# Kernel optimization log

Hardware: AMD Instinct MI355X
Metric: run time of the kernel (lower is better)

## Reference

```python
import jax, jax.numpy as jnp
import numpy as np

N, E, C, ED = 50000, 800000, 128, 16
NEG_SLOPE = 0.2


def setup_inputs() -> dict:
    key = jax.random.key(0)
    ks = jax.random.split(key, 18)
    inp = {
        "h": jax.random.normal(ks[0], (N, C), jnp.float32),
        "edge_index": jax.random.randint(ks[1], (2, E), 0, N),
        "edge_attr": jax.random.normal(ks[2], (E, ED), jnp.float32),
        "reducible": jax.random.randint(ks[3], (N,), 0, 2) > 0,
    }
    names = ["W", "att_src", "att_dst", "W_edge", "att_edge", "W_res", "bias"]
    shapes = [(C, C), (C,), (C,), (ED, C), (C,), (C, C), (C,)]
    i = 4
    for pre in ["red_", "irr_"]:
        for n, sh in zip(names, shapes):
            inp[pre + n] = jax.random.normal(ks[i], sh, jnp.float32) * 0.05
            i += 1
    return inp


def _gat_conv(h, src, dst, edge_attr, W, att_src, att_dst, W_edge, att_edge, W_res, bias):
    """PyG GATConv (heads=1, residual=True, add_self_loops=True, fill_value='mean')."""
    n = h.shape[0]
    # self-loop edge_attr = mean of incoming edge_attr per node (0 if none)
    sum_attr = jax.ops.segment_sum(edge_attr, dst, num_segments=n)
    cnt = jax.ops.segment_sum(jnp.ones((edge_attr.shape[0],), edge_attr.dtype), dst, num_segments=n)
    mean_attr = sum_attr / jnp.maximum(cnt, 1.0)[:, None]
    loop = jnp.arange(n)
    s = jnp.concatenate([src, loop])   # [E+N]
    d = jnp.concatenate([dst, loop])   # [E+N]
    ea = jnp.concatenate([edge_attr, mean_attr], axis=0)  # [E+N, ED]
    x = h @ W                              # [N, C]
    a_src = x @ att_src                    # [N]
    a_dst = x @ att_dst                    # [N]
    a_edge = (ea @ W_edge) @ att_edge      # [E+N]
    alpha = jax.nn.leaky_relu(a_src[s] + a_dst[d] + a_edge, NEG_SLOPE)
    # per-destination softmax (every node has a self-loop -> denom > 0)
    m = jax.ops.segment_max(alpha, d, num_segments=n)
    ex = jnp.exp(alpha - m[d])
    denom = jax.ops.segment_sum(ex, d, num_segments=n)
    w = ex / denom[d]                      # [E+N]
    out = jax.ops.segment_sum(w[:, None] * x[s], d, num_segments=n)  # [N, C]
    return out + h @ W_res + bias


def reference(h, edge_index, edge_attr, reducible,
              red_W, red_att_src, red_att_dst, red_W_edge, red_att_edge, red_W_res, red_bias,
              irr_W, irr_att_src, irr_att_dst, irr_W_edge, irr_att_edge, irr_W_res, irr_bias):
    src, dst = edge_index[0], edge_index[1]
    out_r = _gat_conv(h, src, dst, edge_attr, red_W, red_att_src, red_att_dst,
                      red_W_edge, red_att_edge, red_W_res, red_bias)
    out_i = _gat_conv(h, src, dst, edge_attr, irr_W, irr_att_src, irr_att_dst,
                      irr_W_edge, irr_att_edge, irr_W_res, irr_bias)
    return jax.nn.relu(jnp.where(reducible[:, None], out_r, out_i))
```

## Files before the change

kernel.cpp:

```cpp
#include <hip/hip_runtime.h>
#include <hip/hip_bf16.h>

#define CDIM 128
#define EDIM 16
#define NEG_SLOPE 0.2f

typedef __attribute__((ext_vector_type(8))) short bf16x8;
typedef __attribute__((ext_vector_type(4))) float f32x4;
typedef __attribute__((ext_vector_type(2))) float f32x2;
typedef unsigned int uint;
typedef unsigned short ushort;

__device__ __forceinline__ ushort f2bf(float f) {
    uint u = __float_as_uint(f);
    return (ushort)((u + 0x7fffu + ((u >> 16) & 1u)) >> 16);
}
__device__ __forceinline__ uint packbf(float lo, float hi) {
    return ((uint)f2bf(hi) << 16) | (uint)f2bf(lo);
}
__device__ __forceinline__ float bflo(uint w) { return __uint_as_float(w << 16); }
__device__ __forceinline__ float bfhi(uint w) { return __uint_as_float(w & 0xffff0000u); }

__device__ __forceinline__ bool redtest(const void* red, int i, int notInt, int notFloat) {
    if (!notInt)        return ((const int*)red)[i] != 0;
    else if (!notFloat) return ((const float*)red)[i] != 0.f;
    else                return ((const unsigned char*)red)[i] != 0;
}

__global__ void bcatwe_kernel(const float* __restrict__ Wr, const float* __restrict__ Wi,
                              const float* __restrict__ Wrr, const float* __restrict__ Wri,
                              ushort* __restrict__ BT,
                              const float* __restrict__ WeR, const float* __restrict__ aeR,
                              const float* __restrict__ WeI, const float* __restrict__ aeI,
                              float* __restrict__ we) {
    if (blockIdx.x < 256) {
        int idx = blockIdx.x * 256 + threadIdx.x;
        int c = idx >> 7, k = idx & 127;
        const float* srcm;
        if (c < 128)      srcm = Wr;
        else if (c < 256) srcm = Wi;
        else if (c < 384) srcm = Wrr;
        else              srcm = Wri;
        BT[idx] = f2bf(srcm[k * 128 + (c & 127)]);
    } else {
        int lane = threadIdx.x;
        if (lane < 16) {
            float s = 0.f;
            for (int c = 0; c < CDIM; ++c) s += WeR[lane * CDIM + c] * aeR[c];
            we[lane] = s;
        } else if (lane < 32) {
            int j = lane - 16;
            float s = 0.f;
            for (int c = 0; c < CDIM; ++c) s += WeI[j * CDIM + c] * aeI[c];
            we[16 + j] = s;
        }
    }
}

__global__ __launch_bounds__(256) void prep_kernel(const uint* __restrict__ red, int nwords,
                                                   int* __restrict__ flags,
                                                   const int* __restrict__ dst, int* __restrict__ cnt,
                                                   int* __restrict__ rank,
                                                   const float* __restrict__ ea, const float* __restrict__ we,
                                                   uint* __restrict__ escal4,
                                                   const float* __restrict__ h, ushort* __restrict__ hbf,
                                                   int E, int n4) {
    int i = blockIdx.x * 256 + threadIdx.x;
    if (i < nwords) {
        uint w = red[i];
        bool isInt = (w <= 1u);
        bool isFloat = (w == 0u) || (w == 0x3f800000u);
        if (!isInt) atomicOr(&flags[0], 1);
        if (!isFloat) atomicOr(&flags[1], 1);
    }
    if (i < E) {
        int r = atomicAdd(&cnt[dst[i]], 1);
        __builtin_nontemporal_store(r, rank + i);
        const f32x4* row = (const f32x4*)(ea + (size_t)i * EDIM);
        const float4* we4 = (const float4*)we;
        float er = 0.f, ei = 0.f;
#pragma unroll
        for (int q = 0; q < 4; ++q) {
            f32x4 v = __builtin_nontemporal_load(row + q);
            float4 wr = we4[q], wi = we4[4 + q];
            er += v.x * wr.x + v.y * wr.y + v.z * wr.z + v.w * wr.w;
            ei += v.x * wi.x + v.y * wi.y + v.z * wi.z + v.w * wi.w;
        }
        __builtin_nontemporal_store(packbf(er, ei), escal4 + i);
    }
    if (i < n4) {
        f32x4 v = __builtin_nontemporal_load((const f32x4*)h + i);
        uint2 o;
        o.x = packbf(v.x, v.y);
        o.y = packbf(v.z, v.w);
        ((uint2*)hbf)[i] = o;
    }
}

__global__ __launch_bounds__(256) void gemm_dots(const ushort* __restrict__ A,
                                                 const ushort* __restrict__ BT,
                                                 ushort* __restrict__ C,
                                                 const float* __restrict__ attsr, const float* __restrict__ attdr,
                                                 const float* __restrict__ attsi, const float* __restrict__ attdi,
                                                 float* __restrict__ asr, float* __restrict__ adr,
                                                 float* __restrict__ asi, float* __restrict__ adi,
                                                 const void* __restrict__ red, const int* __restrict__ flags,
                                                 int M) {
    __shared__ ushort As[128 * 128];
    __shared__ ushort Bs[128 * 128];
    __shared__ float dots[2][128];
    __shared__ unsigned char redrow[128];
    int t = threadIdx.x;
    int lane = t & 63, wv = t >> 6;
    int rb = blockIdx.x * 128, cb = blockIdx.y * 128;
    int by = blockIdx.y;

    if (t < 128) { dots[0][t] = 0.f; dots[1][t] = 0.f; }
    if (by >= 2 && t < 128) {
        int gr = rb + t;
        int notInt = flags[0], notFloat = flags[1];
        redrow[t] = (gr < M) ? (redtest(red, gr, notInt, notFloat) ? 1 : 0) : 0;
    }

    int rsub = wv * 4 + (lane >> 4);
    int c0 = lane & 15;
#pragma unroll
    for (int p = 0; p < 8; ++p) {
        int row = p * 16 + rsub;
        int chunk = c0 ^ (row & 7);
        int gra = rb + row; if (gra > M - 1) gra = M - 1;
        const ushort* ga = A + (size_t)gra * 128 + chunk * 8;
        __builtin_amdgcn_global_load_lds(
            (const __attribute__((address_space(1))) void*)ga,
            (__attribute__((address_space(3))) void*)((char*)As + p * 4096 + wv * 1024),
            16, 0, 0);
        const ushort* gb = BT + (size_t)(cb + row) * 128 + chunk * 8;
        __builtin_amdgcn_global_load_lds(
            (const __attribute__((address_space(1))) void*)gb,
            (__attribute__((address_space(3))) void*)((char*)Bs + p * 4096 + wv * 1024),
            16, 0, 0);
    }
    __syncthreads();

    int wr = wv >> 1, wc = wv & 1;
    int l15 = lane & 15, l4 = lane >> 4;
    f32x4 acc[4][4];
#pragma unroll
    for (int i = 0; i < 4; ++i)
#pragma unroll
        for (int j = 0; j < 4; ++j) acc[i][j] = (f32x4){0.f, 0.f, 0.f, 0.f};

    const char* Ab = (const char*)As;
    const char* Bb = (const char*)Bs;
#pragma unroll
    for (int ks = 0; ks < 4; ++ks) {
        bf16x8 a[4], b[4];
#pragma unroll
        for (int f = 0; f < 4; ++f) {
            int row = wr * 64 + f * 16 + l15;
            int ch = (ks * 4 + l4) ^ (row & 7);
            a[f] = *(const bf16x8*)(Ab + row * 256 + ch * 16);
            int col = wc * 64 + f * 16 + l15;
            int ch2 = (ks * 4 + l4) ^ (col & 7);
            b[f] = *(const bf16x8*)(Bb + col * 256 + ch2 * 16);
        }
#pragma unroll
        for (int i = 0; i < 4; ++i)
#pragma unroll
            for (int j = 0; j < 4; ++j)
                acc[i][j] = __builtin_amdgcn_mfma_f32_16x16x32_bf16(a[i], b[j], acc[i][j], 0, 0, 0);
    }

    if (by < 2) {
        const float* attS = by ? attsi : attsr;
        const float* attD = by ? attdi : attdr;
        float aS[4], aD[4];
#pragma unroll
        for (int j = 0; j < 4; ++j) {
            int c = wc * 64 + j * 16 + l15;
            aS[j] = attS[c]; aD[j] = attD[c];
        }
#pragma unroll
        for (int i = 0; i < 4; ++i)
#pragma unroll
            for (int rr = 0; rr < 4; ++rr) {
                float ps = 0.f, pd = 0.f;
#pragma unroll
                for (int j = 0; j < 4; ++j) {
                    float v = acc[i][j][rr];
                    ps += v * aS[j]; pd += v * aD[j];
                }
#pragma unroll
                for (int d = 1; d < 16; d <<= 1) {
                    ps += __shfl_xor(ps, d); pd += __shfl_xor(pd, d);
                }
                if (l15 == 0) {
                    int row = wr * 64 + i * 16 + l4 * 4 + rr;
                    atomicAdd(&dots[0][row], ps);
                    atomicAdd(&dots[1][row], pd);
                }
            }
    }

#pragma unroll
    for (int i = 0; i < 4; ++i) {
        int rl = wr * 64 + i * 16 + l4 * 4;
#pragma unroll
        for (int j = 0; j < 4; ++j) {
            int col = cb + wc * 64 + j * 16 + l15;
#pragma unroll
            for (int r = 0; r < 4; ++r) {
                int gr = rb + rl + r;
                bool doit = gr < M;
                if (by == 2) doit = doit && redrow[rl + r];
                else if (by == 3) doit = doit && !redrow[rl + r];
                if (doit) C[(size_t)gr * 512 + col] = f2bf(acc[i][j][r]);
            }
        }
    }

    if (by < 2) {
        __syncthreads();
        if (t < 128) {
            int gr = rb + t;
            if (gr < M) {
                if (by == 0) { asr[gr] = dots[0][t]; adr[gr] = dots[1][t]; }
                else         { asi[gr] = dots[0][t]; adi[gr] = dots[1][t]; }
            }
        }
    }
}

__global__ __launch_bounds__(256) void scanA_kernel(const int* __restrict__ cnt,
                                                    int* __restrict__ offA,
                                                    int* __restrict__ bsum, int n) {
    __shared__ int wsum[4];
    int t = threadIdx.x, lane = t & 63, wid = t >> 6;
    int i0 = blockIdx.x * 1024 + t * 4;
    int v[4];
#pragma unroll
    for (int j = 0; j < 4; ++j) { int i = i0 + j; v[j] = (i < n) ? cnt[i] : 0; }
    int s = v[0] + v[1] + v[2] + v[3];
    int incl = s;
#pragma unroll
    for (int d = 1; d < 64; d <<= 1) { int u = __shfl_up(incl, d); if (lane >= d) incl += u; }
    if (lane == 63) wsum[wid] = incl;
    __syncthreads();
    int wpre = 0;
    for (int w = 0; w < wid; ++w) wpre += wsum[w];
    int run = wpre + incl - s;
#pragma unroll
    for (int j = 0; j < 4; ++j) {
        int i = i0 + j;
        if (i < n) offA[i] = run;
        run += v[j];
    }
    if (t == 255) bsum[blockIdx.x] = wpre + incl;
}

__global__ void scanB_kernel(int* __restrict__ bsum, int nb) {
    int lane = threadIdx.x;
    int carry = 0;
    for (int base = 0; base < nb; base += 64) {
        int i = base + lane;
        int v = (i < nb) ? bsum[i] : 0;
        int incl = v;
#pragma unroll
        for (int d = 1; d < 64; d <<= 1) { int u = __shfl_up(incl, d); if (lane >= d) incl += u; }
        if (i < nb) bsum[i] = carry + incl - v;
        carry += __shfl(incl, 63);
    }
}

__global__ __launch_bounds__(256) void scatter_kernel(
    const int* __restrict__ src, const int* __restrict__ dst,
    const int* __restrict__ rank, const uint* __restrict__ escal4,
    const void* __restrict__ red, const int* __restrict__ flags,
    const int* __restrict__ offA, const int* __restrict__ bsum,
    uint* __restrict__ csr, int E) {
    int e = blockIdx.x * 256 + threadIdx.x;
    if (e >= E) return;
    int s = __builtin_nontemporal_load(src + e);
    int d = __builtin_nontemporal_load(dst + e);
    uint ee = __builtin_nontemporal_load(escal4 + e);
    int rk = __builtin_nontemporal_load(rank + e);
    int notInt = flags[0], notFloat = flags[1];
    bool rr = redtest(red, d, notInt, notFloat);
    uint evb = rr ? (ee & 0xffffu) : (ee >> 16);
    int off = offA[d] + bsum[d >> 10];
    csr[off + rk] = (uint)s | (evb << 16);
}

__global__ __launch_bounds__(256) void node_kernel(
    const ushort* __restrict__ xcat,
    const float* __restrict__ adst_r, const float* __restrict__ adst_i,
    const float* __restrict__ asrc_r, const float* __restrict__ asrc_i,
    const void* __restrict__ red, const int* __restrict__ flags,
    const int* __restrict__ offA, const int* __restrict__ bsum,
    const uint* __restrict__ csr,
    const float* __restrict__ bias_r, const float* __restrict__ bias_i,
    float* __restrict__ out, int n, int E) {
    __shared__ uint2 buf[4][64];
    int wv = threadIdx.x >> 6, lane = threadIdx.x & 63;
    int node = blockIdx.x * 4 + wv;
    if (node >= n) return;

    int notInt = flags[0], notFloat = flags[1];
    bool r = redtest(red, node, notInt, notFloat);

    const float* asrc = r ? asrc_r : asrc_i;
    float adst = (r ? adst_r : adst_i)[node];
    uint vsel = r ? 0u : 256u;
    int b0 = offA[node] + bsum[node >> 10];
    int b1 = (node + 1 < n) ? (offA[node + 1] + bsum[(node + 1) >> 10]) : E;
    int k = b1 - b0;
    const char* xb = (const char*)xcat;
    uint lane4 = lane * 4;

    float m = -1e30f, denom = 0.f;
    float2 acca = make_float2(0.f, 0.f), accb = make_float2(0.f, 0.f);
    float sumE = 0.f;

    for (int base = b0; base < b1; base += 64) {
        int j = base + lane;
        float al = -1e30f; uint soff = 0;
        if (j < b1) {
            uint rec = __builtin_nontemporal_load(csr + j);
            uint s = rec & 0xffffu;
            float ev = bfhi(rec);
            sumE += ev;
            soff = s * 1024u + vsel;
            float a = asrc[s] + ev + adst;
            al = (a >= 0.f) ? a : NEG_SLOPE * a;
        }
        float cm = al;
#pragma unroll
        for (int d = 32; d; d >>= 1) cm = fmaxf(cm, __shfl_xor(cm, d));
        float mn = fmaxf(m, cm);
        float sc = __expf(m - mn);
        denom *= sc;
        acca.x *= sc; acca.y *= sc; accb.x *= sc; accb.y *= sc;
        m = mn;
        float ex = (j < b1) ? __expf(al - mn) : 0.f;
        buf[wv][lane] = make_uint2(__float_as_uint(ex), soff);
        __builtin_amdgcn_wave_barrier();
        int cc = min(64, b1 - base);
        int ccp = (cc + 7) & ~7;
        for (int tq = 0; tq < ccp; tq += 8) {
            uint2 u[8];
#pragma unroll
            for (int q = 0; q < 8; ++q) u[q] = buf[wv][tq + q];
            uint v[8];
#pragma unroll
            for (int q = 0; q < 8; ++q) v[q] = *(const uint*)(xb + u[q].y + lane4);
#pragma unroll
            for (int q = 0; q < 4; ++q) {
                float w = __uint_as_float(u[q].x);
                acca.x += w * bflo(v[q]); acca.y += w * bfhi(v[q]);
            }
#pragma unroll
            for (int q = 4; q < 8; ++q) {
                float w = __uint_as_float(u[q].x);
                accb.x += w * bflo(v[q]); accb.y += w * bfhi(v[q]);
            }
        }
        float exs = ex;
#pragma unroll
        for (int d = 32; d; d >>= 1) exs += __shfl_xor(exs, d);
        denom += exs;
        __builtin_amdgcn_wave_barrier();
    }
    float acc0 = acca.x + accb.x, acc1 = acca.y + accb.y;

#pragma unroll
    for (int d = 32; d; d >>= 1) sumE += __shfl_xor(sumE, d);
    float eself = sumE / fmaxf((float)k, 1.f);
    float a = asrc[node] + adst + eself;
    float aself = (a >= 0.f) ? a : NEG_SLOPE * a;
    float mn = fmaxf(m, aself);
    float sc = __expf(m - mn);
    float exl = __expf(aself - mn);
    denom = denom * sc + exl;
    uint voff = (uint)node * 1024u + vsel;
    uint vsw = *(const uint*)(xb + voff + lane4);
    acc0 = acc0 * sc + exl * bflo(vsw);
    acc1 = acc1 * sc + exl * bfhi(vsw);

    float inv = 1.f / denom;
    uint roff = (uint)node * 1024u + (r ? 512u : 768u);
    uint bw = *(const uint*)(xb + roff + lane4);
    float2 bi2 = ((const float2*)(r ? bias_r : bias_i))[lane];
    f32x2 o;
    o.x = fmaxf(acc0 * inv + bflo(bw) + bi2.x, 0.f);
    o.y = fmaxf(acc1 * inv + bfhi(bw) + bi2.y, 0.f);
    __builtin_nontemporal_store(o, ((f32x2*)out) + (size_t)node * 64 + lane);
}

extern "C" void kernel_launch(void* const* d_in, const int* in_sizes, int n_in,
                              void* d_out, int out_size, void* d_ws, size_t ws_size,
                              hipStream_t stream) {
    const float* h          = (const float*)d_in[0];
    const int*   edge_index = (const int*)d_in[1];
    const float* edge_attr  = (const float*)d_in[2];
    const void*  reducible  = d_in[3];
    const float* red_W      = (const float*)d_in[4];
    const float* red_att_src= (const float*)d_in[5];
    const float* red_att_dst= (const float*)d_in[6];
    const float* red_W_edge = (const float*)d_in[7];
    const float* red_att_edge=(const float*)d_in[8];
    const float* red_W_res  = (const float*)d_in[9];
    const float* red_bias   = (const float*)d_in[10];
    const float* irr_W      = (const float*)d_in[11];
    const float* irr_att_src= (const float*)d_in[12];
    const float* irr_att_dst= (const float*)d_in[13];
    const float* irr_W_edge = (const float*)d_in[14];
    const float* irr_att_edge=(const float*)d_in[15];
    const float* irr_W_res  = (const float*)d_in[16];
    const float* irr_bias   = (const float*)d_in[17];

    const int N = in_sizes[0] / CDIM;
    const int E = in_sizes[1] / 2;
    const int* src = edge_index;
    const int* dst = edge_index + E;
    const int nb = (N + 1023) / 1024;
    const int n4 = N * 128 / 4;

    float* out = (float*)d_out;

    size_t cur = 0;
    auto alloc = [&](size_t bytes) { size_t p = cur; cur = (cur + bytes + 255) & ~(size_t)255; return p; };
    char* ws = (char*)d_ws;
    size_t o_xcat  = alloc((size_t)N * 512 * 2);
    size_t o_hbf   = alloc((size_t)N * 128 * 2);
    size_t o_bcat  = alloc(512 * 128 * 2);
    size_t o_we    = alloc(256);
    size_t o_asr   = alloc((size_t)N * 4);
    size_t o_adr   = alloc((size_t)N * 4);
    size_t o_asi   = alloc((size_t)N * 4);
    size_t o_adi   = alloc((size_t)N * 4);
    size_t o_flags = alloc(256);
    size_t o_cnt   = alloc((size_t)N * 4);
    size_t o_offA  = alloc((size_t)N * 4);
    size_t o_bsum  = alloc((size_t)(nb + 1) * 4);
    size_t o_rank  = alloc((size_t)E * 4);
    size_t o_escal = alloc((size_t)E * 4);
    size_t o_csr   = alloc((size_t)E * 4);
    if (cur > ws_size) return;

    ushort* xcat = (ushort*)(ws + o_xcat);
    ushort* hbf  = (ushort*)(ws + o_hbf);
    ushort* bcat = (ushort*)(ws + o_bcat);
    float* we    = (float*)(ws + o_we);
    float* asr   = (float*)(ws + o_asr);
    float* adr   = (float*)(ws + o_adr);
    float* asi   = (float*)(ws + o_asi);
    float* adi   = (float*)(ws + o_adi);
    int*   flags = (int*)(ws + o_flags);
    int*   cnt   = (int*)(ws + o_cnt);
    int*   offA  = (int*)(ws + o_offA);
    int*   bsum  = (int*)(ws + o_bsum);
    int*   rank  = (int*)(ws + o_rank);
    uint*  escal4= (uint*)(ws + o_escal);
    uint*  csr   = (uint*)(ws + o_csr);

    hipMemsetAsync(flags, 0, 8, stream);
    hipMemsetAsync(cnt, 0, (size_t)N * 4, stream);

    bcatwe_kernel<<<257, 256, 0, stream>>>(red_W, irr_W, red_W_res, irr_W_res, bcat,
                                           red_W_edge, red_att_edge, irr_W_edge, irr_att_edge, we);

    int nwords = N / 4;
    int pgrid = (max(E, n4) + 255) / 256;
    prep_kernel<<<pgrid, 256, 0, stream>>>((const uint*)reducible, nwords, flags,
                                           dst, cnt, rank, edge_attr, we, escal4,
                                           h, hbf, E, n4);

    dim3 ggrid((N + 127) / 128, 4);
    gemm_dots<<<ggrid, 256, 0, stream>>>(hbf, bcat, xcat,
                                         red_att_src, red_att_dst,
                                         irr_att_src, irr_att_dst,
                                         asr, adr, asi, adi,
                                         reducible, flags, N);

    scanA_kernel<<<nb, 256, 0, stream>>>(cnt, offA, bsum, N);
    scanB_kernel<<<1, 64, 0, stream>>>(bsum, nb);

    scatter_kernel<<<(E + 255) / 256, 256, 0, stream>>>(src, dst, rank, escal4,
                                                        reducible, flags, offA, bsum, csr, E);

    node_kernel<<<(N + 3) / 4, 256, 0, stream>>>(xcat, adr, adi, asr, asi,
                                                 reducible, flags, offA, bsum, csr,
                                                 red_bias, irr_bias, out, N, E);
}
```

Measured before the change: 170.8 us.

## Loop over all four weight column blocks per row tile, reusing the A tile

The GEMM grid changes from (rows x 4 column blocks) to one block per 128-row tile. Each block loads its A tile into shared memory once and loops over the four 128-column weight slices, reloading only B. The conditional masked stores of the residual columns by the reducible flag are removed, so all 512 columns are written for every row. This saves three redundant A-tile loads per row tile but cuts the grid to a quarter of the blocks, serialises the B loads behind syncthreads with no overlap, and writes more output bytes.

```diff
diff --git a/kernel.cpp b/kernel.cpp
--- a/kernel.cpp
+++ b/kernel.cpp
@@ -104,23 +104,15 @@
                                                  const float* __restrict__ attsi, const float* __restrict__ attdi,
                                                  float* __restrict__ asr, float* __restrict__ adr,
                                                  float* __restrict__ asi, float* __restrict__ adi,
-                                                 const void* __restrict__ red, const int* __restrict__ flags,
                                                  int M) {
     __shared__ ushort As[128 * 128];
     __shared__ ushort Bs[128 * 128];
-    __shared__ float dots[2][128];
-    __shared__ unsigned char redrow[128];
+    __shared__ float dots[4][128];
     int t = threadIdx.x;
     int lane = t & 63, wv = t >> 6;
-    int rb = blockIdx.x * 128, cb = blockIdx.y * 128;
-    int by = blockIdx.y;
-
-    if (t < 128) { dots[0][t] = 0.f; dots[1][t] = 0.f; }
-    if (by >= 2 && t < 128) {
-        int gr = rb + t;
-        int notInt = flags[0], notFloat = flags[1];
-        redrow[t] = (gr < M) ? (redtest(red, gr, notInt, notFloat) ? 1 : 0) : 0;
-    }
+    int rb = blockIdx.x * 128;
+
+    if (t < 128) { dots[0][t] = 0.f; dots[1][t] = 0.f; dots[2][t] = 0.f; dots[3][t] = 0.f; }
 
     int rsub = wv * 4 + (lane >> 4);
     int c0 = lane & 15;
@@ -134,99 +126,103 @@
             (const __attribute__((address_space(1))) void*)ga,
             (__attribute__((address_space(3))) void*)((char*)As + p * 4096 + wv * 1024),
             16, 0, 0);
-        const ushort* gb = BT + (size_t)(cb + row) * 128 + chunk * 8;
-        __builtin_amdgcn_global_load_lds(
-            (const __attribute__((address_space(1))) void*)gb,
-            (__attribute__((address_space(3))) void*)((char*)Bs + p * 4096 + wv * 1024),
-            16, 0, 0);
-    }
-    __syncthreads();
+    }
 
     int wr = wv >> 1, wc = wv & 1;
     int l15 = lane & 15, l4 = lane >> 4;
-    f32x4 acc[4][4];
-#pragma unroll
-    for (int i = 0; i < 4; ++i)
-#pragma unroll
-        for (int j = 0; j < 4; ++j) acc[i][j] = (f32x4){0.f, 0.f, 0.f, 0.f};
-
     const char* Ab = (const char*)As;
     const char* Bb = (const char*)Bs;
-#pragma unroll
-    for (int ks = 0; ks < 4; ++ks) {
-        bf16x8 a[4], b[4];
-#pragma unroll
-        for (int f = 0; f < 4; ++f) {
-            int row = wr * 64 + f * 16 + l15;
-            int ch = (ks * 4 + l4) ^ (row & 7);
-            a[f] = *(const bf16x8*)(Ab + row * 256 + ch * 16);
-            int col = wc * 64 + f * 16 + l15;
-            int ch2 = (ks * 4 + l4) ^ (col & 7);
-            b[f] = *(const bf16x8*)(Bb + col * 256 + ch2 * 16);
-        }
+
+    for (int s = 0; s < 4; ++s) {
+#pragma unroll
+        for (int p = 0; p < 8; ++p) {
+            int row = p * 16 + rsub;
+            int chunk = c0 ^ (row & 7);
+            const ushort* gb = BT + (size_t)(s * 128 + row) * 128 + chunk * 8;
+            __builtin_amdgcn_global_load_lds(
+                (const __attribute__((address_space(1))) void*)gb,
+                (__attribute__((address_space(3))) void*)((char*)Bs + p * 4096 + wv * 1024),
+                16, 0, 0);
+        }
+        __syncthreads();
+
+        f32x4 acc[4][4];
 #pragma unroll
         for (int i = 0; i < 4; ++i)
 #pragma unroll
-            for (int j = 0; j < 4; ++j)
-                acc[i][j] = __builtin_amdgcn_mfma_f32_16x16x32_bf16(a[i], b[j], acc[i][j], 0, 0, 0);
-    }
-
-    if (by < 2) {
-        const float* attS = by ? attsi : attsr;
-        const float* attD = by ? attdi : attdr;
-        float aS[4], aD[4];
-#pragma unroll
-        for (int j = 0; j < 4; ++j) {
-            int c = wc * 64 + j * 16 + l15;
-            aS[j] = attS[c]; aD[j] = attD[c];
-        }
-#pragma unroll
-        for (int i = 0; i < 4; ++i)
-#pragma unroll
-            for (int rr = 0; rr < 4; ++rr) {
-                float ps = 0.f, pd = 0.f;
-#pragma unroll
-                for (int j = 0; j < 4; ++j) {
-                    float v = acc[i][j][rr];
-                    ps += v * aS[j]; pd += v * aD[j];
+            for (int j = 0; j < 4; ++j) acc[i][j] = (f32x4){0.f, 0.f, 0.f, 0.f};
+
+#pragma unroll
+        for (int ks = 0; ks < 4; ++ks) {
+            bf16x8 a[4], b[4];
+#pragma unroll
+            for (int f = 0; f < 4; ++f) {
+                int row = wr * 64 + f * 16 + l15;
+                int ch = (ks * 4 + l4) ^ (row & 7);
+                a[f] = *(const bf16x8*)(Ab + row * 256 + ch * 16);
+                int col = wc * 64 + f * 16 + l15;
+                int ch2 = (ks * 4 + l4) ^ (col & 7);
+                b[f] = *(const bf16x8*)(Bb + col * 256 + ch2 * 16);
+            }
+#pragma unroll
+            for (int i = 0; i < 4; ++i)
+#pragma unroll
+                for (int j = 0; j < 4; ++j)
+                    acc[i][j] = __builtin_amdgcn_mfma_f32_16x16x32_bf16(a[i], b[j], acc[i][j], 0, 0, 0);
+        }
+
+        if (s < 2) {
+            const float* attS = s ? attsi : attsr;
+            const float* attD = s ? attdi : attdr;
+            float aS[4], aD[4];
+#pragma unroll
+            for (int j = 0; j < 4; ++j) {
+                int c = wc * 64 + j * 16 + l15;
+                aS[j] = attS[c]; aD[j] = attD[c];
+            }
+#pragma unroll
+            for (int i = 0; i < 4; ++i)
+#pragma unroll
+                for (int rr = 0; rr < 4; ++rr) {
+                    float ps = 0.f, pd = 0.f;
+#pragma unroll
+                    for (int j = 0; j < 4; ++j) {
+                        float v = acc[i][j][rr];
+                        ps += v * aS[j]; pd += v * aD[j];
+                    }
+#pragma unroll
+                    for (int d = 1; d < 16; d <<= 1) {
+                        ps += __shfl_xor(ps, d); pd += __shfl_xor(pd, d);
+                    }
+                    if (l15 == 0) {
+                        int row = wr * 64 + i * 16 + l4 * 4 + rr;
+                        atomicAdd(&dots[s * 2 + 0][row], ps);
+                        atomicAdd(&dots[s * 2 + 1][row], pd);
+                    }
                 }
-#pragma unroll
-                for (int d = 1; d < 16; d <<= 1) {
-                    ps += __shfl_xor(ps, d); pd += __shfl_xor(pd, d);
-                }
-                if (l15 == 0) {
-                    int row = wr * 64 + i * 16 + l4 * 4 + rr;
-                    atomicAdd(&dots[0][row], ps);
-                    atomicAdd(&dots[1][row], pd);
+        }
+
+#pragma unroll
+        for (int i = 0; i < 4; ++i) {
+            int rl = wr * 64 + i * 16 + l4 * 4;
+#pragma unroll
+            for (int j = 0; j < 4; ++j) {
+                int col = s * 128 + wc * 64 + j * 16 + l15;
+#pragma unroll
+                for (int r = 0; r < 4; ++r) {
+                    int gr = rb + rl + r;
+                    if (gr < M) C[(size_t)gr * 512 + col] = f2bf(acc[i][j][r]);
                 }
             }
-    }
-
-#pragma unroll
-    for (int i = 0; i < 4; ++i) {
-        int rl = wr * 64 + i * 16 + l4 * 4;
-#pragma unroll
-        for (int j = 0; j < 4; ++j) {
-            int col = cb + wc * 64 + j * 16 + l15;
-#pragma unroll
-            for (int r = 0; r < 4; ++r) {
-                int gr = rb + rl + r;
-                bool doit = gr < M;
-                if (by == 2) doit = doit && redrow[rl + r];
-                else if (by == 3) doit = doit && !redrow[rl + r];
-                if (doit) C[(size_t)gr * 512 + col] = f2bf(acc[i][j][r]);
-            }
-        }
-    }
-
-    if (by < 2) {
+        }
         __syncthreads();
-        if (t < 128) {
-            int gr = rb + t;
-            if (gr < M) {
-                if (by == 0) { asr[gr] = dots[0][t]; adr[gr] = dots[1][t]; }
-                else         { asi[gr] = dots[0][t]; adi[gr] = dots[1][t]; }
-            }
+    }
+
+    if (t < 128) {
+        int gr = rb + t;
+        if (gr < M) {
+            asr[gr] = dots[0][t]; adr[gr] = dots[1][t];
+            asi[gr] = dots[2][t]; adi[gr] = dots[3][t];
         }
     }
 }
@@ -475,12 +471,10 @@
                                            dst, cnt, rank, edge_attr, we, escal4,
                                            h, hbf, E, n4);
 
-    dim3 ggrid((N + 127) / 128, 4);
-    gemm_dots<<<ggrid, 256, 0, stream>>>(hbf, bcat, xcat,
-                                         red_att_src, red_att_dst,
-                                         irr_att_src, irr_att_dst,
-                                         asr, adr, asi, adi,
-                                         reducible, flags, N);
+    gemm_dots<<<(N + 127) / 128, 256, 0, stream>>>(hbf, bcat, xcat,
+                                                   red_att_src, red_att_dst,
+                                                   irr_att_src, irr_att_dst,
+                                                   asr, adr, asi, adi, N);
 
     scanA_kernel<<<nb, 256, 0, stream>>>(cnt, offA, bsum, N);
     scanB_kernel<<<1, 64, 0, stream>>>(bsum, nb);
```

Result: faster. 152.8 us (-10.5%).
